# Kernel tuning notes

Hardware: AMD Instinct MI355X
Metric: run time of the kernel (lower is better)

Reference implementation:

```python
import jax, jax.numpy as jnp
import numpy as np

WIRES = 4
DIM = 16  # 2**WIRES
EPS = 1e-5


def _rot_matrix(phi, theta, omega):
    # PennyLane Rot = RZ(omega) RY(theta) RZ(phi)
    c = jnp.cos(theta / 2).astype(jnp.complex64)
    s = jnp.sin(theta / 2).astype(jnp.complex64)
    ep = jnp.exp(-0.5j * (phi + omega).astype(jnp.complex64))
    em = jnp.exp(0.5j * (phi - omega).astype(jnp.complex64))
    m00 = ep * c
    m01 = -em * s
    m10 = jnp.conj(em) * s
    m11 = jnp.conj(ep) * c
    return jnp.stack([jnp.stack([m00, m01]), jnp.stack([m10, m11])])


def _apply_1q(state4, U, w):
    # state4: (B,2,2,2,2); apply 2x2 unitary on wire w (axis w+1)
    st = jnp.moveaxis(state4, w + 1, -1)
    st = st @ U.T  # sum_j st[...,j] * U[i,j]
    return jnp.moveaxis(st, -1, w + 1)


def _cnot_perm(c, t):
    # permutation of 16 basis indices for CNOT(control=c, target=t); wire 0 = MSB
    idx = np.arange(DIM)
    cbit = (idx >> (WIRES - 1 - c)) & 1
    return idx ^ (cbit << (WIRES - 1 - t))


def _circuit(x16, params):
    # AmplitudeEmbedding with normalize=True
    B = x16.shape[0]
    nrm = jnp.linalg.norm(x16, axis=1, keepdims=True)
    state = (x16 / nrm).astype(jnp.complex64)  # (B,16)
    L = params.shape[0]
    for l in range(L):
        st4 = state.reshape(B, 2, 2, 2, 2)
        for w in range(WIRES):
            U = _rot_matrix(params[l, w, 0], params[l, w, 1], params[l, w, 2])
            st4 = _apply_1q(st4, U, w)
        state = st4.reshape(B, DIM)
        r = (l % (WIRES - 1)) + 1  # StronglyEntanglingLayers default range
        for w in range(WIRES):
            perm = _cnot_perm(w, (w + r) % WIRES)
            state = state[:, perm]
    probs = (state.real ** 2 + state.imag ** 2)  # (B,16)
    p4 = probs.reshape(B, 2, 2, 2, 2)
    # <Z_w> = P(bit_w=0) - P(bit_w=1)
    outs = []
    for w in range(WIRES):
        axes = tuple(a for a in range(1, 5) if a != w + 1)
        pw = p4.sum(axis=axes)  # (B,2)
        outs.append(pw[:, 0] - pw[:, 1])
    return jnp.stack(outs, axis=1)  # (B,4)


def setup_inputs() -> dict:
    key = jax.random.key(0)
    k1, k2 = jax.random.split(key)
    B = 65536
    x = jax.random.normal(k1, (B, 1, 24, 24), dtype=jnp.float32)
    params = jax.random.normal(k2, (2, WIRES, 3), dtype=jnp.float32)
    gamma = jnp.ones((WIRES,), dtype=jnp.float32)
    beta = jnp.zeros((WIRES,), dtype=jnp.float32)
    return {"x": x, "params": params, "gamma": gamma, "beta": beta}


def reference(x, params, gamma, beta):
    B = x.shape[0]
    # avg_pool2d kernel 6: (B,1,24,24) -> (B,1,4,4) -> (B,16)
    pooled = x.reshape(B, 1, 4, 6, 4, 6).mean(axis=(3, 5)).reshape(B, DIM)
    out = _circuit(pooled, params)  # (B,4)
    # BatchNorm1d in training mode (biased batch stats)
    mu = out.mean(axis=0)
    var = ((out - mu) ** 2).mean(axis=0)
    return (out - mu) / jnp.sqrt(var + EPS) * gamma + beta
```

## Files before the change

kernel.cpp:

```cpp
#include <hip/hip_runtime.h>
#include <math.h>

#define BATCH 65536
#define XPER  576
#define NBLK  512
#define EPB   128
#define WPB   4
#define IPW   (EPB / WPB)
#define CHUNK 4
#define NCH   (IPW / CHUNK)
#define CHF   (CHUNK * XPER)


__device__ __forceinline__ void gload16(const float* g, float* l) {
    __builtin_amdgcn_global_load_lds(
        (__attribute__((address_space(1))) void*)(g),
        (__attribute__((address_space(3))) void*)(l),
        16, 0, 0);
}

__global__ __launch_bounds__(256, 2) void circuit_kernel(
        const float* __restrict__ x, const float* __restrict__ params,
        float* __restrict__ out, float* __restrict__ accums) {
    __shared__ float sx[WPB][2][CHF];
    __shared__ float sU[512];
    __shared__ float sg[48];
    __shared__ float sv[256];
    __shared__ float spart[8];

    const int t    = threadIdx.x;
    const int wid  = t >> 6;
    const int lane = t & 63;
    const int e    = lane >> 4;
    const int p    = lane & 15;

    const size_t ibase = (size_t)blockIdx.x * EPB + (size_t)wid * IPW;

    {
        const float* src = x + ibase * XPER + lane * 4;
        float* dst = &sx[wid][0][0];
#pragma unroll
        for (int j = 0; j < 9; ++j) gload16(src + j * 256, dst + j * 256);
    }

    if (t < 8) {
        spart[t] = 0.0f;
        float phi   = params[t * 3 + 0];
        float theta = params[t * 3 + 1];
        float omega = params[t * 3 + 2];
        float apo = 0.5f * (phi + omega), amo = 0.5f * (phi - omega);
        sg[t * 6 + 0] = cosf(0.5f * theta);
        sg[t * 6 + 1] = sinf(0.5f * theta);
        sg[t * 6 + 2] = cosf(apo);
        sg[t * 6 + 3] = -sinf(apo);
        sg[t * 6 + 4] = cosf(amo);
        sg[t * 6 + 5] = sinf(amo);
    }
    __syncthreads();

    if (t < 16) {
        const int j = t;
        float Mr[16], Mi[16];
#pragma unroll
        for (int i = 0; i < 16; ++i) { Mr[i] = (i == j) ? 1.0f : 0.0f; Mi[i] = 0.0f; }
#pragma unroll
        for (int l = 0; l < 2; ++l) {
#pragma unroll
            for (int w = 0; w < 4; ++w) {
                const int g = l * 4 + w;
                float c   = sg[g * 6 + 0], s   = sg[g * 6 + 1];
                float epr = sg[g * 6 + 2], epi = sg[g * 6 + 3];
                float emr = sg[g * 6 + 4], emi = sg[g * 6 + 5];
                float m00r =  epr * c, m00i =  epi * c;
                float m01r = -emr * s, m01i = -emi * s;
                float m10r =  emr * s, m10i = -emi * s;
                float m11r =  epr * c, m11i = -epi * c;
                const int mask = 1 << (3 - w);
#pragma unroll
                for (int i = 0; i < 16; ++i) {
                    if (i & mask) continue;
                    int i1 = i | mask;
                    float r0 = Mr[i],  q0 = Mi[i];
                    float r1 = Mr[i1], q1 = Mi[i1];
                    Mr[i]  = m00r * r0 - m00i * q0 + m01r * r1 - m01i * q1;
                    Mi[i]  = m00r * q0 + m00i * r0 + m01r * q1 + m01i * r1;
                    Mr[i1] = m10r * r0 - m10i * q0 + m11r * r1 - m11i * q1;
                    Mi[i1] = m10r * q0 + m10i * r0 + m11r * q1 + m11i * r1;
                }
            }
            const int rr = (l % 3) + 1;
#pragma unroll
            for (int w = 0; w < 4; ++w) {
                int tq = (w + rr) & 3;
                int cb = 3 - w, tb = 3 - tq;
#pragma unroll
                for (int i = 0; i < 16; ++i) {
                    int pi = i ^ (((i >> cb) & 1) << tb);
                    if (pi > i) {
                        float tr = Mr[i]; Mr[i] = Mr[pi]; Mr[pi] = tr;
                        float ti = Mi[i]; Mi[i] = Mi[pi]; Mi[pi] = ti;
                    }
                }
            }
        }
#pragma unroll
        for (int i = 0; i < 16; ++i) {
            sU[i * 16 + j]       = Mr[i];
            sU[256 + i * 16 + j] = Mi[i];
        }
    }
    __syncthreads();

    float ur[16], ui[16];
    {
        const float4* u4 = (const float4*)(sU + p * 16);
        const float4* v4 = (const float4*)(sU + 256 + p * 16);
#pragma unroll
        for (int q = 0; q < 4; ++q) {
            float4 a = u4[q], b = v4[q];
            ur[4 * q + 0] = a.x; ur[4 * q + 1] = a.y; ur[4 * q + 2] = a.z; ur[4 * q + 3] = a.w;
            ui[4 * q + 0] = b.x; ui[4 * q + 1] = b.y; ui[4 * q + 2] = b.z; ui[4 * q + 3] = b.w;
        }
    }

    int c = -1;
    if      (p == 8) c = 0;
    else if (p == 4) c = 1;
    else if (p == 2) c = 2;
    else if (p == 1) c = 3;

    const int r0 = (e + (p >> 2)) % 6;
    float zbuf[NCH];
    float accz = 0.0f, accz2 = 0.0f;

#pragma unroll
    for (int ch = 0; ch < NCH; ++ch) {
        if (ch + 1 < NCH) {
            const float* src = x + (ibase + (size_t)(ch + 1) * CHUNK) * XPER + lane * 4;
            float* dst = &sx[wid][(ch + 1) & 1][0];
#pragma unroll
            for (int j = 0; j < 9; ++j) gload16(src + j * 256, dst + j * 256);
            asm volatile("s_waitcnt vmcnt(9)" ::: "memory");
        } else {
            asm volatile("s_waitcnt vmcnt(0)" ::: "memory");
        }

        const float* bs = &sx[wid][ch & 1][0] + e * XPER + (p >> 2) * 144 + (p & 3) * 6;
        float sum = 0.0f;
#pragma unroll
        for (int i = 0; i < 6; ++i) {
            int row = r0 + i; if (row >= 6) row -= 6;
            const float2* rp = (const float2*)(bs + row * 24);
            float2 a2 = rp[0], b2 = rp[1], d2 = rp[2];
            sum += a2.x + a2.y + b2.x + b2.y + d2.x + d2.y;
        }
        float v = sum * (1.0f / 36.0f);

        sv[wid * 64 + e * 16 + p] = v;
        float vv[16];
        {
            const float4* vb = (const float4*)(sv + wid * 64 + e * 16);
#pragma unroll
            for (int q = 0; q < 4; ++q) {
                float4 a = vb[q];
                vv[4 * q + 0] = a.x; vv[4 * q + 1] = a.y;
                vv[4 * q + 2] = a.z; vv[4 * q + 3] = a.w;
            }
        }
        float n2 = 0.0f, sr = 0.0f, si = 0.0f;
#pragma unroll
        for (int j = 0; j < 16; ++j) {
            n2 = fmaf(vv[j], vv[j], n2);
            sr = fmaf(ur[j], vv[j], sr);
            si = fmaf(ui[j], vv[j], si);
        }
        float prob = (sr * sr + si * si) / n2;

        float a = prob, o;
        o = __shfl_xor(a, 1); a = (t & 1) ? (o - a) : (a + o);
        o = __shfl_xor(a, 2); a = (t & 2) ? (o - a) : (a + o);
        o = __shfl_xor(a, 4); a = (t & 4) ? (o - a) : (a + o);
        o = __shfl_xor(a, 8); a = (t & 8) ? (o - a) : (a + o);

        zbuf[ch] = a;
        if (c >= 0) { accz += a; accz2 += a * a; }
    }

    if (c >= 0) {
#pragma unroll
        for (int ch = 0; ch < NCH; ++ch)
            out[(ibase + (size_t)ch * CHUNK + e) * 4 + c] = zbuf[ch];
        atomicAdd(&spart[c], accz);
        atomicAdd(&spart[4 + c], accz2);
    }
    __syncthreads();
    if (t < 8) atomicAdd(&accums[t], spart[t]);
}

__global__ __launch_bounds__(256) void bn_apply(float* __restrict__ out,
                                                const float* __restrict__ accums,
                                                const float* __restrict__ gamma,
                                                const float* __restrict__ beta) {
    __shared__ float sc[8];
    const int t = threadIdx.x;
    if (t < 4) {
        float mu  = accums[t] * (1.0f / BATCH);
        float var = accums[4 + t] * (1.0f / BATCH) - mu * mu;
        float a = gamma[t] * rsqrtf(var + 1e-5f);
        sc[t]     = a;
        sc[4 + t] = beta[t] - mu * a;
    }
    __syncthreads();
    int i = blockIdx.x * 256 + t;
    float4 z = ((float4*)out)[i];
    z.x = fmaf(z.x, sc[0], sc[4]);
    z.y = fmaf(z.y, sc[1], sc[5]);
    z.z = fmaf(z.z, sc[2], sc[6]);
    z.w = fmaf(z.w, sc[3], sc[7]);
    ((float4*)out)[i] = z;
}

extern "C" void kernel_launch(void* const* d_in, const int* in_sizes, int n_in,
                              void* d_out, int out_size, void* d_ws, size_t ws_size,
                              hipStream_t stream) {
    const float* x      = (const float*)d_in[0];
    const float* params = (const float*)d_in[1];
    const float* gamma  = (const float*)d_in[2];
    const float* beta   = (const float*)d_in[3];
    float* out = (float*)d_out;
    float* ws  = (float*)d_ws;

    hipMemsetAsync(ws, 0, 32, stream);
    hipLaunchKernelGGL(circuit_kernel, dim3(NBLK), dim3(256), 0, stream,
                       x, params, out, ws);
    hipLaunchKernelGGL(bn_apply, dim3(BATCH / 256), dim3(256), 0, stream,
                       out, ws, gamma, beta);
}
```

Baseline: 40.66 us.

## Permute LDS staging layout so pooling reads use aligned float4 loads

The global-to-LDS async copy now scatters each 16-byte segment into a permuted LDS layout grouped by pooling patch-pair, so each thread can read its 6x6 window with aligned float4 LDS loads instead of float2 loads. The 12-wide pair of patches is split between two lanes, which share partial sums through a lane shuffle. This targets LDS read instruction count and bank conflicts in the pooling step. In exchange, global reads become non-contiguous per lane (a 16-byte gather with precomputed offsets), which may hurt coalescing, and it adds one shuffle.

```diff
diff --git a/kernel.cpp b/kernel.cpp
--- a/kernel.cpp
+++ b/kernel.cpp
@@ -12,6 +12,7 @@
 #define CHF   (CHUNK * XPER)
 
 
+
 __device__ __forceinline__ void gload16(const float* g, float* l) {
     __builtin_amdgcn_global_load_lds(
         (__attribute__((address_space(1))) void*)(g),
@@ -36,11 +37,23 @@
 
     const size_t ibase = (size_t)blockIdx.x * EPB + (size_t)wid * IPW;
 
+    int goff[9];
+#pragma unroll
+    for (int j = 0; j < 9; ++j) {
+        int Lf  = j * 256 + lane * 4;
+        int q   = Lf / 72;
+        int rem = Lf - q * 72;
+        int rr  = rem / 12;
+        int mm  = rem - rr * 12;
+        int e2 = q >> 3, pr2 = (q >> 1) & 3, P2 = q & 1;
+        goff[j] = e2 * 576 + (pr2 * 6 + rr) * 24 + P2 * 12 + mm;
+    }
+
     {
-        const float* src = x + ibase * XPER + lane * 4;
+        const float* xb = x + ibase * XPER;
         float* dst = &sx[wid][0][0];
 #pragma unroll
-        for (int j = 0; j < 9; ++j) gload16(src + j * 256, dst + j * 256);
+        for (int j = 0; j < 9; ++j) gload16(xb + goff[j], dst + j * 256);
     }
 
     if (t < 8) {
@@ -123,38 +136,62 @@
         }
     }
 
+    const int prow = p >> 2, pc = p & 3;
+    const int P = pc >> 1, s = pc & 1;
+    const int qa = (e << 3) + (prow << 1) + P;
+    const int rbase = qa * 72;
+    const int r0 = qa % 6;
+    int offF[6], offS[3];
+#pragma unroll
+    for (int k = 0; k < 6; ++k) {
+        int rk = r0 + k; if (rk >= 6) rk -= 6;
+        offF[k] = rbase + rk * 12 + (s ? 8 : 0);
+    }
+#pragma unroll
+    for (int k = 0; k < 3; ++k) {
+        int rk = r0 + 3 * s + k; if (rk >= 6) rk -= 6;
+        offS[k] = rbase + rk * 12 + 4;
+    }
+
     int c = -1;
     if      (p == 8) c = 0;
     else if (p == 4) c = 1;
     else if (p == 2) c = 2;
     else if (p == 1) c = 3;
 
-    const int r0 = (e + (p >> 2)) % 6;
     float zbuf[NCH];
     float accz = 0.0f, accz2 = 0.0f;
 
 #pragma unroll
     for (int ch = 0; ch < NCH; ++ch) {
         if (ch + 1 < NCH) {
-            const float* src = x + (ibase + (size_t)(ch + 1) * CHUNK) * XPER + lane * 4;
+            const float* xb = x + (ibase + (size_t)(ch + 1) * CHUNK) * XPER;
             float* dst = &sx[wid][(ch + 1) & 1][0];
 #pragma unroll
-            for (int j = 0; j < 9; ++j) gload16(src + j * 256, dst + j * 256);
+            for (int j = 0; j < 9; ++j) gload16(xb + goff[j], dst + j * 256);
             asm volatile("s_waitcnt vmcnt(9)" ::: "memory");
         } else {
             asm volatile("s_waitcnt vmcnt(0)" ::: "memory");
         }
 
-        const float* bs = &sx[wid][ch & 1][0] + e * XPER + (p >> 2) * 144 + (p & 3) * 6;
-        float sum = 0.0f;
-#pragma unroll
-        for (int i = 0; i < 6; ++i) {
-            int row = r0 + i; if (row >= 6) row -= 6;
-            const float2* rp = (const float2*)(bs + row * 24);
-            float2 a2 = rp[0], b2 = rp[1], d2 = rp[2];
-            sum += a2.x + a2.y + b2.x + b2.y + d2.x + d2.y;
-        }
-        float v = sum * (1.0f / 36.0f);
+        const float* bb = &sx[wid][ch & 1][0];
+        float accFull = 0.0f, accLs = 0.0f, accRs = 0.0f;
+#pragma unroll
+        for (int k = 0; k < 6; ++k) {
+            float4 a = *(const float4*)(bb + offF[k]);
+            accFull += a.x + a.y + a.z + a.w;
+        }
+#pragma unroll
+        for (int k = 0; k < 3; ++k) {
+            float4 a = *(const float4*)(bb + offS[k]);
+            accLs += a.x + a.y;
+            accRs += a.z + a.w;
+        }
+        float myL = s ? accLs : (accFull + accLs);
+        float myR = s ? (accFull + accRs) : accRs;
+        float send = s ? myL : myR;
+        float recv = __shfl_xor(send, 1);
+        float v = ((s ? myR : myL) + recv) * (1.0f / 36.0f);
 
         sv[wid * 64 + e * 16 + p] = v;
         float vv[16];
```

New measurement: 40.51 us. No clear change (-0.4%).
